# Kernel tuning notes

Measured on AMD Instinct MI355X. Metric: run time of the kernel, lower is better.

The kernel has to match this reference:

```python
import jax, jax.numpy as jnp
import numpy as np

N_ = 512   # batch / num users
M_ = 254   # num UAV nodes -> size S = M_ + 2 = 256
D_ = 2     # coordinate dim
H_ = 128   # pointer-net hidden dim


def setup_inputs() -> dict:
    key = jax.random.key(0)
    ks = jax.random.split(key, 7)
    s = 0.1
    return {
        "outputs": jax.random.normal(ks[0], (2 * N_ + M_, D_), dtype=jnp.float32),
        "W_embed": jax.random.normal(ks[1], (D_, H_), dtype=jnp.float32) * s,
        "b_embed": jnp.zeros((H_,), jnp.float32),
        "lstm_Wi": jax.random.normal(ks[2], (H_, 4 * H_), dtype=jnp.float32) * s,
        "lstm_Wh": jax.random.normal(ks[3], (H_, 4 * H_), dtype=jnp.float32) * s,
        "lstm_b": jnp.zeros((4 * H_,), jnp.float32),
        "att_W1": jax.random.normal(ks[4], (H_, H_), dtype=jnp.float32) * s,
        "att_W2": jax.random.normal(ks[5], (H_, H_), dtype=jnp.float32) * s,
        "att_v": jax.random.normal(ks[6], (H_,), dtype=jnp.float32) * s,
        "N": N_,
    }


def _rgnn_loss(outputs, W_embed, b_embed, lstm_Wi, lstm_Wh, lstm_b,
               att_W1, att_W2, att_v, N):
    D = outputs.shape[1]
    H = W_embed.shape[1]
    M = outputs.shape[0] - 2 * N
    users_src = outputs[:N][:, None, :]                         # (B,1,D)
    users_dst = outputs[N:2 * N][:, None, :]                    # (B,1,D)
    uav_nodes = jnp.broadcast_to(outputs[2 * N:][None, :, :], (N, M, D))
    uav_graph = jnp.concatenate([users_src, uav_nodes, users_dst], axis=1)  # (B,S,D)
    B, S = uav_graph.shape[0], uav_graph.shape[1]
    NEG = jnp.float32(-np.inf)

    # pointer-net: node embeddings and step-independent attention projection
    e_all = uav_graph @ W_embed + b_embed                       # (B,S,H)
    W1e = jnp.einsum('bsh,hk->bsk', e_all, att_W1)              # (B,S,H)
    rows = jnp.arange(B)

    mask0 = jnp.zeros((B, S), jnp.float32).at[:, 0].set(NEG)
    x0 = uav_graph[:, 0, :]                                     # start at src
    carry0 = (x0, x0,
              jnp.zeros((B, H), jnp.float32), jnp.zeros((B, H), jnp.float32),
              mask0, jnp.zeros((B,), jnp.float32))

    def step(carry, k):
        x, Y0, h, c, mask, max_dist = carry
        # dst node blocked only at step 0, re-opened afterwards
        mask = mask.at[:, -1].set(jnp.where(k == 0, NEG, 0.0))
        # LSTM cell on embedded current node
        e_x = x @ W_embed + b_embed                             # (B,H)
        gates = e_x @ lstm_Wi + h @ lstm_Wh + lstm_b            # (B,4H)
        i, f, g, o = jnp.split(gates, 4, axis=1)
        c = jax.nn.sigmoid(f) * c + jax.nn.sigmoid(i) * jnp.tanh(g)
        h = jax.nn.sigmoid(o) * jnp.tanh(c)
        # additive attention pointer logits
        q = h @ att_W2                                          # (B,H)
        logits = jnp.tanh(W1e + q[:, None, :]) @ att_v + mask   # (B,S)
        logits = jax.lax.stop_gradient(logits)                  # output.detach()
        idx = jnp.argmax(logits, axis=1)                        # (B,)
        Y1 = uav_graph[rows, idx]                               # (B,D)
        dist = jnp.sqrt(jnp.sum((Y1 - Y0) ** 2, axis=1) + 1e-12)
        max_dist = jnp.maximum(max_dist, dist)
        mask = mask.at[rows, idx].add(NEG)
        mask = jnp.where((idx == S)[:, None], NEG, mask)
        return (Y1, Y1, h, c, mask, max_dist), None

    (_, _, _, _, _, max_dist), _ = jax.lax.scan(step, carry0, jnp.arange(S))
    return max_dist.mean()


def reference(outputs, W_embed, b_embed, lstm_Wi, lstm_Wh, lstm_b,
              att_W1, att_W2, att_v, N):
    return _rgnn_loss(outputs, W_embed, b_embed, lstm_Wi, lstm_Wh, lstm_b,
                      att_W1, att_W2, att_v, N)
```

## Files before the change

kernel.cpp:

```cpp
#include <hip/hip_runtime.h>
#include <math.h>

#define NB   512
#define MM   254
#define SS   256
#define HH   128
#define RTOT 1278
#define NBLK 256

#define C2   2.885390081777927f
#define C1   1.442695040888963f

__device__ __forceinline__ float rcpf(float x)  { return __builtin_amdgcn_rcpf(x); }
__device__ __forceinline__ float exp2f_(float x){ return __builtin_amdgcn_exp2f(x); }
__device__ __forceinline__ float sigm2(float x) { return rcpf(1.0f + exp2f_(-C1 * x)); }
__device__ __forceinline__ float tanh2(float x) { return 1.0f - 2.0f * rcpf(1.0f + exp2f_(C2 * x)); }

__global__ __launch_bounds__(512) void coef_k(
    const float* __restrict__ Wemb, const float* __restrict__ bemb,
    const float* __restrict__ Wi, const float* __restrict__ W1,
    const float* __restrict__ lb, float* __restrict__ coef)
{
  int j = threadIdx.x;
  float a = 0.f, b = 0.f, c = 0.f;
#pragma unroll 8
  for (int h = 0; h < HH; ++h) {
    float w = Wi[(size_t)h * 512 + j];
    a = fmaf(Wemb[h], w, a);
    b = fmaf(Wemb[HH + h], w, b);
    c = fmaf(bemb[h], w, c);
  }
  coef[j] = a; coef[512 + j] = b; coef[1024 + j] = c + lb[j];
  if (j < HH) {
    float a1 = 0.f, b1 = 0.f, c1 = 0.f;
#pragma unroll 8
    for (int h = 0; h < HH; ++h) {
      float w = W1[(size_t)h * HH + j];
      a1 = fmaf(Wemb[h], w, a1);
      b1 = fmaf(Wemb[HH + h], w, b1);
      c1 = fmaf(bemb[h], w, c1);
    }
    coef[1536 + j] = C2 * a1; coef[1664 + j] = C2 * b1; coef[1792 + j] = C2 * c1;
  }
}

__global__ __launch_bounds__(128) void transpose_k(
    const float* __restrict__ Wh, const float* __restrict__ W2,
    float* __restrict__ WhT, float* __restrict__ W2T)
{
  int bidx = blockIdx.x;
  int k = threadIdx.x;
  if (bidx < 512) WhT[(size_t)bidx * 128 + k] = Wh[(size_t)k * 512 + bidx];
  else {
    int j = bidx - 512;
    W2T[(size_t)j * 128 + k] = W2[(size_t)k * 128 + j];
  }
}

__global__ __attribute__((amdgpu_waves_per_eu(4, 4)))
__launch_bounds__(1024) void decode_k(
    const float* __restrict__ outputs, const float* __restrict__ WhT,
    const float* __restrict__ Wh, const float* __restrict__ W2T,
    const float* __restrict__ av, const float* __restrict__ coef,
    float* __restrict__ maxd_out)
{
  const int t = threadIdx.x;
  const int bid = blockIdx.x;

  __shared__ float WhL[64][512];
  __shared__ float posU[2 * MM];
  __shared__ float dstS[2][2];
  __shared__ float curP[2][2];
  __shared__ __align__(16) float hS[2][HH];
  __shared__ __align__(16) float qC[2][HH];
  __shared__ __align__(16) float vS2[HH];
  __shared__ float sumvS[2];
  __shared__ __align__(16) float AiS[512], BiS[512], CiS[512];
  __shared__ __align__(16) float A1sS[HH], B1sS[HH], C1sS[HH];
  __shared__ float pS[2][2][512];
  __shared__ float lp[2][2][SS];
  __shared__ int   lsS[2][SS];
  __shared__ int   actS[2][254];
  __shared__ int   cntS[2];

  const int gh  = (t >> 5) & 1;
  const int gj  = ((t >> 6) << 5) | (t & 31);
  const int cg  = t >> 9;
  const int cj  = (t >> 2) & 127;
  const int ckq = t & 3;
  const int lg  = t >> 9;
  const int lhf = (t >> 8) & 1;
  const int lu  = t & 255;

  float4 whreg[8];
  {
    const float4* wg4 = (const float4*)(WhT + (size_t)gj * 128 + gh * 32);
#pragma unroll
    for (int i = 0; i < 8; ++i) whreg[i] = wg4[i];
  }

  for (int i = t; i < 64 * 512; i += 1024) ((float*)WhL)[i] = Wh[64 * 512 + i];
  for (int i = t; i < 2 * MM; i += 1024)   posU[i] = outputs[4 * NB + i];
  if (t < 512) { AiS[t] = coef[t]; BiS[t] = coef[512 + t]; CiS[t] = coef[1024 + t]; }
  if (t < HH)  { A1sS[t] = coef[1536 + t]; B1sS[t] = coef[1664 + t]; C1sS[t] = coef[1792 + t]; }
  if (t < 256) { int gg = t >> 7, j = t & 127; hS[gg][j] = 0.f; }
  if (t < HH) vS2[t] = -2.0f * av[t];
  if (t >= 256 && t < 258) {
    int half = t - 256; float s = 0.f;
    for (int h = half * 64; h < half * 64 + 64; ++h) s += av[h];
    sumvS[half] = s;
  }
  if (t < 254) actS[0][t] = t + 1;
  else if (t >= 512 && t < 766) actS[1][t - 512] = t - 511;
  if (t == 0) {
    cntS[0] = 254;
    dstS[0][0] = outputs[2 * (NB + bid)]; dstS[0][1] = outputs[2 * (NB + bid) + 1];
    curP[0][0] = outputs[2 * bid];        curP[0][1] = outputs[2 * bid + 1];
  }
  if (t == 512) {
    cntS[1] = 254;
    dstS[1][0] = outputs[2 * (NB + bid + NBLK)];
    dstS[1][1] = outputs[2 * (NB + bid + NBLK) + 1];
    curP[1][0] = outputs[2 * (bid + NBLK)];
    curP[1][1] = outputs[2 * (bid + NBLK) + 1];
  }
  __syncthreads();

  float px = 0.f, py = 0.f, md = 0.f;
  if (t == 0)   { px = curP[0][0]; py = curP[0][1]; }
  if (t == 512) { px = curP[1][0]; py = curP[1][1]; }

  float creg = 0.f;

  for (int k = 0; k < SS; ++k) {
    {
      float a0G = 0.f, a1G = 0.f, a0L = 0.f, a1L = 0.f;
      {
        const float* wl = &WhL[gh * 32][gj];
        const float4* hb0 = (const float4*)(&hS[0][64 + gh * 32]);
        const float4* hb1 = (const float4*)(&hS[1][64 + gh * 32]);
#pragma unroll
        for (int i = 0; i < 8; ++i) {
          float4 h0 = hb0[i], h1 = hb1[i];
          float wa = wl[(size_t)(4 * i) * 512];
          float wbv = wl[(size_t)(4 * i + 1) * 512];
          float wc = wl[(size_t)(4 * i + 2) * 512];
          float wd = wl[(size_t)(4 * i + 3) * 512];
          a0L = fmaf(h0.x, wa, a0L); a0L = fmaf(h0.y, wbv, a0L);
          a0L = fmaf(h0.z, wc, a0L); a0L = fmaf(h0.w, wd, a0L);
          a1L = fmaf(h1.x, wa, a1L); a1L = fmaf(h1.y, wbv, a1L);
          a1L = fmaf(h1.z, wc, a1L); a1L = fmaf(h1.w, wd, a1L);
        }
      }
      {
        const float4* hb0 = (const float4*)(&hS[0][gh * 32]);
        const float4* hb1 = (const float4*)(&hS[1][gh * 32]);
#pragma unroll
        for (int i = 0; i < 8; ++i) {
          float4 h0 = hb0[i], h1 = hb1[i];
          float4 w = whreg[i];
          a0G = fmaf(h0.x, w.x, a0G); a0G = fmaf(h0.y, w.y, a0G);
          a0G = fmaf(h0.z, w.z, a0G); a0G = fmaf(h0.w, w.w, a0G);
          a1G = fmaf(h1.x, w.x, a1G); a1G = fmaf(h1.y, w.y, a1G);
          a1G = fmaf(h1.z, w.z, a1G); a1G = fmaf(h1.w, w.w, a1G);
        }
      }
      pS[0][gh][gj] = a0G + a0L;
      pS[1][gh][gj] = a1G + a1L;
    }
    __syncthreads();

    if (t < 256) {
      int g = t >> 7, jj = t & 127;
      float pxc = curP[g][0], pyc = curP[g][1];
      float ei = fmaf(pxc, AiS[jj],       fmaf(pyc, BiS[jj],       CiS[jj]))       + (pS[g][0][jj]       + pS[g][1][jj]);
      float ef = fmaf(pxc, AiS[128 + jj], fmaf(pyc, BiS[128 + jj], CiS[128 + jj])) + (pS[g][0][128 + jj] + pS[g][1][128 + jj]);
      float eg = fmaf(pxc, AiS[256 + jj], fmaf(pyc, BiS[256 + jj], CiS[256 + jj])) + (pS[g][0][256 + jj] + pS[g][1][256 + jj]);
      float eo = fmaf(pxc, AiS[384 + jj], fmaf(pyc, BiS[384 + jj], CiS[384 + jj])) + (pS[g][0][384 + jj] + pS[g][1][384 + jj]);
      float iv = sigm2(ei), fv = sigm2(ef), gv = tanh2(eg), ov = sigm2(eo);
      float cn = fv * creg + iv * gv;
      creg = cn;
      hS[g][jj] = ov * tanh2(cn);
    }
    __syncthreads();

    {
      const float4* w4 = (const float4*)(W2T + (size_t)cj * 128 + ckq * 32);
      const float4* h4 = (const float4*)(&hS[cg][ckq * 32]);
      float p0 = 0.f, p1 = 0.f;
#pragma unroll
      for (int i = 0; i < 8; ++i) {
        float4 w = w4[i], h = h4[i];
        p0 = fmaf(h.x, w.x, p0); p1 = fmaf(h.y, w.y, p1);
        p0 = fmaf(h.z, w.z, p0); p1 = fmaf(h.w, w.w, p1);
      }
      float p = p0 + p1;
      p += __shfl_xor(p, 1);
      p += __shfl_xor(p, 2);
      if (ckq == 0) qC[cg][cj] = fmaf(C2, p, C1sS[cj]);
    }
    __syncthreads();

    {
      int cnt = cntS[lg];
      int cntEff = cnt + (k > 0 ? 1 : 0);
      if (lu < cntEff) {
        int s = (lu == cnt) ? 255 : actS[lg][lu];
        float pxn, pyn;
        if (s == 255) { pxn = dstS[lg][0]; pyn = dstS[lg][1]; }
        else          { pxn = posU[2 * (s - 1)]; pyn = posU[2 * (s - 1) + 1]; }
        const float4* a14 = (const float4*)(&A1sS[lhf * 64]);
        const float4* b14 = (const float4*)(&B1sS[lhf * 64]);
        const float4* qc4 = (const float4*)(&qC[lg][lhf * 64]);
        const float4* vv4 = (const float4*)(&vS2[lhf * 64]);
        float c0 = 0.f, c1 = 0.f;
#pragma unroll 4
        for (int i = 0; i < 16; ++i) {
          float4 a = a14[i], b = b14[i], qc = qc4[i], v = vv4[i];
          float wx = fmaf(pxn, a.x, fmaf(pyn, b.x, qc.x));
          float wy = fmaf(pxn, a.y, fmaf(pyn, b.y, qc.y));
          float wz = fmaf(pxn, a.z, fmaf(pyn, b.z, qc.z));
          float ww = fmaf(pxn, a.w, fmaf(pyn, b.w, qc.w));
          c0 = fmaf(v.x, rcpf(1.0f + exp2f_(wx)), c0);
          c1 = fmaf(v.y, rcpf(1.0f + exp2f_(wy)), c1);
          c0 = fmaf(v.z, rcpf(1.0f + exp2f_(wz)), c0);
          c1 = fmaf(v.w, rcpf(1.0f + exp2f_(ww)), c1);
        }
        lp[lg][lhf][lu] = (c0 + c1) + sumvS[lhf];
        if (lhf == 0) lsS[lg][lu] = s;
      }
    }
    __syncthreads();

    if ((t < 64) || (t >= 512 && t < 576)) {
      int g = t >> 9;
      int lane = t & 63;
      int cnt = cntS[g];
      int cntEff = cnt + (k > 0 ? 1 : 0);
      float val = -INFINITY;
      unsigned key = 0xFFFFFFFFu;
#pragma unroll
      for (int c = 0; c < 4; ++c) {
        int u = lane + 64 * c;
        if (u < cntEff) {
          float v2 = lp[g][0][u] + lp[g][1][u];
          unsigned k2 = ((unsigned)lsS[g][u] << 16) | (unsigned)u;
          if (v2 > val || (v2 == val && k2 < key)) { val = v2; key = k2; }
        }
      }
#pragma unroll
      for (int off = 1; off < 64; off <<= 1) {
        float v2 = __shfl_xor(val, off);
        unsigned k2 = __shfl_xor(key, off);
        if (v2 > val || (v2 == val && k2 < key)) { val = v2; key = k2; }
      }
      if (lane == 0) {
        int s   = (int)(key >> 16);
        int pos = (int)(key & 0xFFFFu);
        float nx, ny;
        if (s == 255) { nx = dstS[g][0]; ny = dstS[g][1]; }
        else          { nx = posU[2 * (s - 1)]; ny = posU[2 * (s - 1) + 1]; }
        float dx = nx - px, dy = ny - py;
        float d = sqrtf(dx * dx + dy * dy + 1e-12f);
        if (d > md) md = d;
        px = nx; py = ny;
        curP[g][0] = nx; curP[g][1] = ny;
        if (s != 255) { actS[g][pos] = actS[g][cnt - 1]; cntS[g] = cnt - 1; }
      }
    }
    __syncthreads();
  }

  if (t == 0)   maxd_out[bid] = md;
  if (t == 512) maxd_out[bid + NBLK] = md;
}

__global__ __launch_bounds__(512) void reduce_k(const float* __restrict__ maxd,
                                               float* __restrict__ out)
{
  __shared__ float s[512];
  int t = threadIdx.x;
  s[t] = maxd[t];
  __syncthreads();
  for (int off = 256; off > 0; off >>= 1) {
    if (t < off) s[t] += s[t + off];
    __syncthreads();
  }
  if (t == 0) out[0] = s[0] * (1.0f / 512.0f);
}

extern "C" void kernel_launch(void* const* d_in, const int* in_sizes, int n_in,
                              void* d_out, int out_size, void* d_ws, size_t ws_size,
                              hipStream_t stream) {
  const float* outputs = (const float*)d_in[0];
  const float* Wemb    = (const float*)d_in[1];
  const float* bemb    = (const float*)d_in[2];
  const float* Wi      = (const float*)d_in[3];
  const float* Wh      = (const float*)d_in[4];
  const float* lb      = (const float*)d_in[5];
  const float* W1      = (const float*)d_in[6];
  const float* W2      = (const float*)d_in[7];
  const float* av      = (const float*)d_in[8];

  float* ws   = (float*)d_ws;
  float* coef = ws;
  float* WhT  = coef + 2048;
  float* W2T  = WhT + (size_t)512 * 128;
  float* maxd = W2T + (size_t)128 * 128;

  hipLaunchKernelGGL(coef_k, dim3(1), dim3(512), 0, stream,
                     Wemb, bemb, Wi, W1, lb, coef);
  hipLaunchKernelGGL(transpose_k, dim3(640), dim3(128), 0, stream, Wh, W2, WhT, W2T);
  hipLaunchKernelGGL(decode_k, dim3(NBLK), dim3(1024), 0, stream,
                     outputs, WhT, Wh, W2T, av, coef, maxd);
  hipLaunchKernelGGL(reduce_k, dim3(1), dim3(512), 0, stream, maxd, (float*)d_out);
}
```

Measured before the change: 2.121 ms.

## Split attention logits across 16-lane groups with register-resident coefficients

Each candidate node's attention score is now computed by a group of 16 lanes. Each lane holds 8 hidden dimensions of the W1 coefficients and v in registers and sums its partial with xor shuffles, replacing the old scheme where one thread looped over 64 dims read from LDS. The LSTM input-projection coefficients also move from shared memory into per-thread registers. The constant sum(v) term is dropped because it does not change the argmax, and the node id is re-derived from actS instead of being stored. This cuts LDS traffic per step but adds shuffles and register pressure under a fixed waves-per-EU limit, which risks spills.

```diff
diff --git a/kernel.cpp b/kernel.cpp
--- a/kernel.cpp
+++ b/kernel.cpp
@@ -73,13 +73,9 @@
   __shared__ float curP[2][2];
   __shared__ __align__(16) float hS[2][HH];
   __shared__ __align__(16) float qC[2][HH];
-  __shared__ __align__(16) float vS2[HH];
-  __shared__ float sumvS[2];
-  __shared__ __align__(16) float AiS[512], BiS[512], CiS[512];
-  __shared__ __align__(16) float A1sS[HH], B1sS[HH], C1sS[HH];
+  __shared__ float C1sS[HH];
   __shared__ float pS[2][2][512];
-  __shared__ float lp[2][2][SS];
-  __shared__ int   lsS[2][SS];
+  __shared__ float lgS[2][SS];
   __shared__ int   actS[2][254];
   __shared__ int   cntS[2];
 
@@ -88,9 +84,12 @@
   const int cg  = t >> 9;
   const int cj  = (t >> 2) & 127;
   const int ckq = t & 3;
-  const int lg  = t >> 9;
-  const int lhf = (t >> 8) & 1;
-  const int lu  = t & 255;
+
+  const int eg  = t >> 9;
+  const int tg  = t & 511;
+  const int ewv = tg >> 6;
+  const int eul = (tg >> 4) & 3;
+  const int esl = tg & 15;
 
   float4 whreg[8];
   {
@@ -98,18 +97,28 @@
 #pragma unroll
     for (int i = 0; i < 8; ++i) whreg[i] = wg4[i];
   }
+  float a_[8], b_[8], v_[8];
+#pragma unroll
+  for (int i = 0; i < 8; ++i) {
+    a_[i] = coef[1536 + esl * 8 + i];
+    b_[i] = coef[1664 + esl * 8 + i];
+    v_[i] = -2.0f * av[esl * 8 + i];
+  }
+  float aI[4], bI[4], cI[4];
+  {
+    int jj = t & 127;
+#pragma unroll
+    for (int c = 0; c < 4; ++c) {
+      aI[c] = coef[c * 128 + jj];
+      bI[c] = coef[512 + c * 128 + jj];
+      cI[c] = coef[1024 + c * 128 + jj];
+    }
+  }
 
   for (int i = t; i < 64 * 512; i += 1024) ((float*)WhL)[i] = Wh[64 * 512 + i];
   for (int i = t; i < 2 * MM; i += 1024)   posU[i] = outputs[4 * NB + i];
-  if (t < 512) { AiS[t] = coef[t]; BiS[t] = coef[512 + t]; CiS[t] = coef[1024 + t]; }
-  if (t < HH)  { A1sS[t] = coef[1536 + t]; B1sS[t] = coef[1664 + t]; C1sS[t] = coef[1792 + t]; }
+  if (t < HH) C1sS[t] = coef[1792 + t];
   if (t < 256) { int gg = t >> 7, j = t & 127; hS[gg][j] = 0.f; }
-  if (t < HH) vS2[t] = -2.0f * av[t];
-  if (t >= 256 && t < 258) {
-    int half = t - 256; float s = 0.f;
-    for (int h = half * 64; h < half * 64 + 64; ++h) s += av[h];
-    sumvS[half] = s;
-  }
   if (t < 254) actS[0][t] = t + 1;
   else if (t >= 512 && t < 766) actS[1][t - 512] = t - 511;
   if (t == 0) {
@@ -173,11 +182,11 @@
     if (t < 256) {
       int g = t >> 7, jj = t & 127;
       float pxc = curP[g][0], pyc = curP[g][1];
-      float ei = fmaf(pxc, AiS[jj],       fmaf(pyc, BiS[jj],       CiS[jj]))       + (pS[g][0][jj]       + pS[g][1][jj]);
-      float ef = fmaf(pxc, AiS[128 + jj], fmaf(pyc, BiS[128 + jj], CiS[128 + jj])) + (pS[g][0][128 + jj] + pS[g][1][128 + jj]);
-      float eg = fmaf(pxc, AiS[256 + jj], fmaf(pyc, BiS[256 + jj], CiS[256 + jj])) + (pS[g][0][256 + jj] + pS[g][1][256 + jj]);
-      float eo = fmaf(pxc, AiS[384 + jj], fmaf(pyc, BiS[384 + jj], CiS[384 + jj])) + (pS[g][0][384 + jj] + pS[g][1][384 + jj]);
-      float iv = sigm2(ei), fv = sigm2(ef), gv = tanh2(eg), ov = sigm2(eo);
+      float ei = fmaf(pxc, aI[0], fmaf(pyc, bI[0], cI[0])) + (pS[g][0][jj]       + pS[g][1][jj]);
+      float ef = fmaf(pxc, aI[1], fmaf(pyc, bI[1], cI[1])) + (pS[g][0][128 + jj] + pS[g][1][128 + jj]);
+      float eg2 = fmaf(pxc, aI[2], fmaf(pyc, bI[2], cI[2])) + (pS[g][0][256 + jj] + pS[g][1][256 + jj]);
+      float eo = fmaf(pxc, aI[3], fmaf(pyc, bI[3], cI[3])) + (pS[g][0][384 + jj] + pS[g][1][384 + jj]);
+      float iv = sigm2(ei), fv = sigm2(ef), gv = tanh2(eg2), ov = sigm2(eo);
       float cn = fv * creg + iv * gv;
       creg = cn;
       hS[g][jj] = ov * tanh2(cn);
@@ -202,32 +211,31 @@
     __syncthreads();
 
     {
-      int cnt = cntS[lg];
+      int cnt = cntS[eg];
       int cntEff = cnt + (k > 0 ? 1 : 0);
-      if (lu < cntEff) {
-        int s = (lu == cnt) ? 255 : actS[lg][lu];
-        float pxn, pyn;
-        if (s == 255) { pxn = dstS[lg][0]; pyn = dstS[lg][1]; }
-        else          { pxn = posU[2 * (s - 1)]; pyn = posU[2 * (s - 1) + 1]; }
-        const float4* a14 = (const float4*)(&A1sS[lhf * 64]);
-        const float4* b14 = (const float4*)(&B1sS[lhf * 64]);
-        const float4* qc4 = (const float4*)(&qC[lg][lhf * 64]);
-        const float4* vv4 = (const float4*)(&vS2[lhf * 64]);
-        float c0 = 0.f, c1 = 0.f;
-#pragma unroll 4
-        for (int i = 0; i < 16; ++i) {
-          float4 a = a14[i], b = b14[i], qc = qc4[i], v = vv4[i];
-          float wx = fmaf(pxn, a.x, fmaf(pyn, b.x, qc.x));
-          float wy = fmaf(pxn, a.y, fmaf(pyn, b.y, qc.y));
-          float wz = fmaf(pxn, a.z, fmaf(pyn, b.z, qc.z));
-          float ww = fmaf(pxn, a.w, fmaf(pyn, b.w, qc.w));
-          c0 = fmaf(v.x, rcpf(1.0f + exp2f_(wx)), c0);
-          c1 = fmaf(v.y, rcpf(1.0f + exp2f_(wy)), c1);
-          c0 = fmaf(v.z, rcpf(1.0f + exp2f_(wz)), c0);
-          c1 = fmaf(v.w, rcpf(1.0f + exp2f_(ww)), c1);
+      float qc_[8];
+#pragma unroll
+      for (int i = 0; i < 8; ++i) qc_[i] = qC[eg][esl * 8 + i];
+#pragma unroll
+      for (int c = 0; c < 8; ++c) {
+        int u = ewv * 4 + eul + 32 * c;
+        if (u < cntEff) {
+          int s = (u == cnt) ? 255 : actS[eg][u];
+          float pxn, pyn;
+          if (s == 255) { pxn = dstS[eg][0]; pyn = dstS[eg][1]; }
+          else          { pxn = posU[2 * (s - 1)]; pyn = posU[2 * (s - 1) + 1]; }
+          float acc = 0.f;
+#pragma unroll
+          for (int i = 0; i < 8; ++i) {
+            float w = fmaf(pxn, a_[i], fmaf(pyn, b_[i], qc_[i]));
+            acc = fmaf(v_[i], rcpf(1.0f + exp2f_(w)), acc);
+          }
+          acc += __shfl_xor(acc, 1);
+          acc += __shfl_xor(acc, 2);
+          acc += __shfl_xor(acc, 4);
+          acc += __shfl_xor(acc, 8);
+          if (esl == 0) lgS[eg][u] = acc;
         }
-        lp[lg][lhf][lu] = (c0 + c1) + sumvS[lhf];
-        if (lhf == 0) lsS[lg][lu] = s;
       }
     }
     __syncthreads();
@@ -243,8 +251,9 @@
       for (int c = 0; c < 4; ++c) {
         int u = lane + 64 * c;
         if (u < cntEff) {
-          float v2 = lp[g][0][u] + lp[g][1][u];
-          unsigned k2 = ((unsigned)lsS[g][u] << 16) | (unsigned)u;
+          float v2 = lgS[g][u];
+          int s = (u == cnt) ? 255 : actS[g][u];
+          unsigned k2 = ((unsigned)s << 16) | (unsigned)u;
           if (v2 > val || (v2 == val && k2 < key)) { val = v2; key = k2; }
         }
       }
```

Result: slower. 3.433 ms (+61.8%).
